# Kernel optimization log

Hardware: AMD Instinct MI355X
Metric: run time of the kernel (lower is better)

## Reference

```python
import jax, jax.numpy as jnp
import numpy as np
from jax import lax

EPS_OT = 0.05
N_ITERS = 100
NEG = -1e9

def _l2norm(x):
    n = jnp.sqrt(jnp.sum(x * x, axis=-1, keepdims=True))
    return x / jnp.maximum(n, 1e-12)

def _sinkhorn(C, mu, nu, mask):
    # C: (B, M, Nq); mu: (B, M); nu: (B, Nq); mask: (B, M) bool
    mrow = mask[:, :, None]   # masks rows of K (B,M,Nq)
    mcol = mask[:, None, :]   # masks cols of K^T (B,Nq,M)
    log_mu = jnp.log(mu + 1e-8)
    log_nu = jnp.log(nu + 1e-8)

    def kernel(u, v):
        return (-C + u[:, :, None] + v[:, None, :]) / EPS_OT

    def step(carry, _):
        u, v = carry
        K = jnp.where(mrow, kernel(u, v), NEG)
        u = EPS_OT * (log_mu - jax.scipy.special.logsumexp(K, axis=2)) + u
        Kt = jnp.where(mcol, jnp.transpose(kernel(u, v), (0, 2, 1)), NEG)
        v = EPS_OT * (log_nu - jax.scipy.special.logsumexp(Kt, axis=2)) + v
        return (u, v), None

    u0 = jnp.zeros_like(mu)
    v0 = jnp.zeros_like(nu)
    (u, v), _ = lax.scan(jax.checkpoint(step), (u0, v0), None, length=N_ITERS)
    K = jnp.where(mrow, kernel(u, v), NEG)
    T = jnp.exp(K)
    return jnp.where(mrow, T, 0.0)

def setup_inputs() -> dict:
    key = jax.random.key(0)
    ks = jax.random.split(key, 12)
    Nq, B, M, C = 1024, 8, 1024, 640
    s = 1.0 / np.sqrt(C)
    return {
        "xq": jax.random.normal(ks[0], (Nq, B, C), jnp.float32),
        "xk": jax.random.normal(ks[1], (B, M, C), jnp.float32),
        "xv": jax.random.normal(ks[2], (B, M, C), jnp.float32),
        "mask": jax.random.randint(ks[3], (B, M), 0, 2).astype(bool),
        "Wq": jax.random.normal(ks[4], (C, C), jnp.float32) * s,
        "bq": jnp.zeros((C,), jnp.float32),
        "Wk": jax.random.normal(ks[5], (C, C), jnp.float32) * s,
        "bk": jnp.zeros((C,), jnp.float32),
        "Wv": jax.random.normal(ks[6], (C, C), jnp.float32) * s,
        "bv": jnp.zeros((C,), jnp.float32),
        "Wp": jax.random.normal(ks[7], (C, C), jnp.float32) * s,
        "bp": jnp.zeros((C,), jnp.float32),
    }

def reference(xq, xk, xv, mask, Wq, bq, Wk, bk, Wv, bv, Wp, bp):
    Nq, B, C = xq.shape
    M = xk.shape[1]
    q = _l2norm(xq @ Wq.T + bq)          # (Nq, B, C)
    k = _l2norm(xk @ Wk.T + bk)          # (B, M, C)
    v = xv @ Wv.T + bv                   # (B, M, C)
    # einsum 'bmc,nbc->bnm' then permute(0,2,1) == direct (B, M, Nq)
    sim = jnp.einsum('bmc,nbc->bmn', k, q)
    wdist = 1.0 - sim
    counts = jnp.sum(mask, axis=1, keepdims=True).astype(sim.dtype)  # (B,1)
    xx = mask.astype(sim.dtype) / jnp.maximum(counts, 1.0)
    xx = jnp.where(counts == 0, 1.0 / M, xx)                         # (B, M)
    yy = jnp.full((B, Nq), 1.0 / Nq, sim.dtype)
    T = _sinkhorn(wdist, xx, yy, mask)                               # (B, M, Nq)
    score_map = (M * Nq) * sim * T
    attn_save = jnp.where(mask, jnp.sum(score_map, axis=-1), 0.0)    # (B, M)
    x = jnp.einsum('bmn,bmc->nbc', T, v)                             # (Nq, B, C)
    out = x @ Wp.T + bp
    return out, attn_save
```

## Files before the change

### kernel.cpp

```cpp
#include <hip/hip_runtime.h>
#include <cstdint>
#include <cstddef>

#define B_DIM 8
#define NQ    1024
#define MK    1024
#define CD    640
#define INV_EPS 20.0f
#define EPS_OT  0.05f

typedef unsigned short u16;
typedef __attribute__((ext_vector_type(8))) short bf16x8;
typedef __attribute__((ext_vector_type(4))) float f32x4;
typedef __attribute__((ext_vector_type(2))) float f32x2;

#define GLDS(gp, lp) __builtin_amdgcn_global_load_lds( \
    (const __attribute__((address_space(1))) void*)(gp), \
    (__attribute__((address_space(3))) void*)(lp), 16, 0, 0)

static __device__ __forceinline__ float wave_reduce_sum(float s) {
#pragma unroll
  for (int off = 32; off; off >>= 1) s += __shfl_xor(s, off, 64);
  return s;
}

static __device__ __forceinline__ u16 f2bf(float f) {
  uint32_t u = __float_as_uint(f);
  u += 0x7fff + ((u >> 16) & 1);
  return (u16)(u >> 16);
}

static __device__ __forceinline__ void g_store(float* p, float v) {
  __hip_atomic_store(p, v, __ATOMIC_RELAXED, __HIP_MEMORY_SCOPE_AGENT);
}
static __device__ __forceinline__ float g_load(const float* p) {
  return __hip_atomic_load((float*)p, __ATOMIC_RELAXED, __HIP_MEMORY_SCOPE_AGENT);
}
static __device__ __forceinline__ void g_storeu(unsigned* p, unsigned v) {
  __hip_atomic_store(p, v, __ATOMIC_RELAXED, __HIP_MEMORY_SCOPE_AGENT);
}
static __device__ __forceinline__ unsigned g_loadu(const unsigned* p) {
  return __hip_atomic_load((unsigned*)p, __ATOMIC_RELAXED, __HIP_MEMORY_SCOPE_AGENT);
}

__global__ void k_setup(const void* __restrict__ maskRaw, int* __restrict__ maskI,
                        float* __restrict__ muVal, float* __restrict__ w,
                        unsigned* __restrict__ ctrl)
{
  __shared__ int s_flag;
  __shared__ int s_cnt[B_DIM];
  const int tid = threadIdx.x;
  if (tid == 0) s_flag = 0;
  if (tid < B_DIM) s_cnt[tid] = 0;
  ctrl[tid] = 0u;
  __syncthreads();

  const unsigned char* mb = (const unsigned char*)maskRaw;
  int local = 0;
  for (int i = tid; i < B_DIM * MK; i += 1024)
    if ((i & 3) && mb[i]) local = 1;
  if (local) atomicOr(&s_flag, 1);
  __syncthreads();

  const int isByte = s_flag;
  const int* mi32 = (const int*)maskRaw;
  for (int i = tid; i < B_DIM * MK; i += 1024) {
    int v = isByte ? (int)mb[i] : mi32[i];
    v = v ? 1 : 0;
    maskI[i] = v;
    if (v) atomicAdd(&s_cnt[i >> 10], 1);
  }
  for (int i = tid; i < B_DIM * NQ; i += 1024) w[i] = 1.0f;
  __syncthreads();
  if (tid < B_DIM) {
    float c = (float)s_cnt[tid];
    muVal[tid] = (c > 0.f ? 1.0f / c : 1.0f / (float)MK) + 1e-8f;
  }
}

__global__ __launch_bounds__(256)
void k_cvt5(const float* __restrict__ x0, u16* __restrict__ d0,
            const float* __restrict__ x1, u16* __restrict__ d1,
            const float* __restrict__ x2, u16* __restrict__ d2,
            const float* __restrict__ x3, u16* __restrict__ d3,
            const float* __restrict__ x4, u16* __restrict__ d4)
{
  const int a = blockIdx.y;
  const float* s; u16* d; int n;
  if      (a == 0) { s = x0; d = d0; n = 8192 * CD; }
  else if (a == 1) { s = x1; d = d1; n = 8192 * CD; }
  else if (a == 2) { s = x2; d = d2; n = 8192 * CD; }
  else if (a == 3) { s = x3; d = d3; n = CD * CD; }
  else             { s = x4; d = d4; n = CD * CD; }
  const int i = (blockIdx.x * 256 + threadIdx.x) * 4;
  if (i >= n) return;
  const float4 v = *(const float4*)(s + i);
  *(ushort4*)(d + i) = make_ushort4(f2bf(v.x), f2bf(v.y), f2bf(v.z), f2bf(v.w));
}

__global__ __launch_bounds__(256)
void k_combineA(const float* __restrict__ Wp, const float* __restrict__ Wv,
                u16* __restrict__ Ah)
{
  __shared__ float Ps[32][68];
  __shared__ float Vs[32][68];
  const int tid = threadIdx.x;
  const int c0 = blockIdx.x << 6, k0 = blockIdx.y << 6;
  const int ty = tid >> 4, tx = tid & 15;
  float acc[4][4];
#pragma unroll
  for (int i = 0; i < 4; ++i)
#pragma unroll
    for (int j = 0; j < 4; ++j) acc[i][j] = 0.f;

  for (int j0 = 0; j0 < CD; j0 += 32) {
    {
      const int c = tid >> 2, j4 = (tid & 3) << 3;
      const float* p = Wp + (size_t)(c0 + c) * CD + j0 + j4;
      float4 u0 = *(const float4*)p, u1 = *(const float4*)(p + 4);
      Ps[j4 + 0][c] = u0.x; Ps[j4 + 1][c] = u0.y; Ps[j4 + 2][c] = u0.z; Ps[j4 + 3][c] = u0.w;
      Ps[j4 + 4][c] = u1.x; Ps[j4 + 5][c] = u1.y; Ps[j4 + 6][c] = u1.z; Ps[j4 + 7][c] = u1.w;
    }
    {
      const int j = tid >> 3, k4 = (tid & 7) << 3;
      const float* p = Wv + (size_t)(j0 + j) * CD + k0 + k4;
      float4 u0 = *(const float4*)p, u1 = *(const float4*)(p + 4);
      *(float4*)&Vs[j][k4] = u0; *(float4*)&Vs[j][k4 + 4] = u1;
    }
    __syncthreads();
#pragma unroll
    for (int j = 0; j < 32; ++j) {
      float a[4], b[4];
      *(float4*)a = *(const float4*)&Ps[j][ty << 2];
      *(float4*)b = *(const float4*)&Vs[j][tx << 2];
#pragma unroll
      for (int i = 0; i < 4; ++i)
#pragma unroll
        for (int jj = 0; jj < 4; ++jj)
          acc[i][jj] = fmaf(a[i], b[jj], acc[i][jj]);
    }
    __syncthreads();
  }
#pragma unroll
  for (int i = 0; i < 4; ++i) {
    *(ushort4*)(Ah + (size_t)(c0 + (ty << 2) + i) * CD + k0 + (tx << 2)) =
      make_ushort4(f2bf(acc[i][0]), f2bf(acc[i][1]), f2bf(acc[i][2]), f2bf(acc[i][3]));
  }
}

__global__ __launch_bounds__(256)
void k_bvp(const float* __restrict__ Wp, const float* __restrict__ bv,
           float* __restrict__ bvp)
{
  const int c = (blockIdx.x << 2) + (threadIdx.x >> 6);
  const int lane = threadIdx.x & 63;
  float s = 0.f;
  for (int j = lane; j < CD; j += 64) s = fmaf(Wp[(size_t)c * CD + j], bv[j], s);
  s = wave_reduce_sum(s);
  if (!lane) bvp[c] = s;
}

__global__ __launch_bounds__(256)
void mfma_proj(const u16* __restrict__ xqh, const u16* __restrict__ xkh,
               const u16* __restrict__ xvh,
               const u16* __restrict__ Wqh, const u16* __restrict__ Wkh,
               const u16* __restrict__ Ah,
               const float* __restrict__ bq, const float* __restrict__ bk,
               const float* __restrict__ bvp,
               float* __restrict__ qb, float* __restrict__ kb,
               float* __restrict__ vp)
{
  __shared__ u16 As[128 * 32];
  __shared__ u16 Bs[128 * 32];
  const int mode = blockIdx.z;
  const u16* X     = (mode == 0) ? xqh : ((mode == 1) ? xkh : xvh);
  const u16* W     = (mode == 0) ? Wqh : ((mode == 1) ? Wkh : Ah);
  const float* bias= (mode == 0) ? bq  : ((mode == 1) ? bk  : bvp);
  float* outp      = (mode == 0) ? qb  : ((mode == 1) ? kb  : vp);

  const int tid = threadIdx.x, wave = tid >> 6, lane = tid & 63;
  const int row0 = blockIdx.x << 7, col0 = blockIdx.y << 7;

  const int rS = (wave << 5) + (lane >> 2);
  const int pc = lane & 3;
  const int kc0 = pc ^ ((rS >> 1) & 3);
  const int kc1 = pc ^ (((rS + 16) >> 1) & 3);
  const u16* gA0 = X + (size_t)(row0 + rS) * CD + (kc0 << 3);
  const u16* gA1 = X + (size_t)(row0 + rS + 16) * CD + (kc1 << 3);
  const u16* gB0 = W + (size_t)(col0 + rS) * CD + (kc0 << 3);
  const u16* gB1 = W + (size_t)(col0 + rS + 16) * CD + (kc1 << 3);
  u16* lA = As + (wave << 10);
  u16* lB = Bs + (wave << 10);

  const int wm0 = (wave & 1) << 6, wn0 = (wave >> 1) << 6;
  int aOff[4], bOff[4];
#pragma unroll
  for (int t = 0; t < 4; ++t) {
    const int ra = wm0 + (t << 4) + (lane & 15);
    aOff[t] = ra * 32 + (((lane >> 4) ^ ((ra >> 1) & 3)) << 3);
    const int rb = wn0 + (t << 4) + (lane & 15);
    bOff[t] = rb * 32 + (((lane >> 4) ^ ((rb >> 1) & 3)) << 3);
  }
  f32x4 acc[4][4];
#pragma unroll
  for (int i = 0; i < 4; ++i)
#pragma unroll
    for (int j = 0; j < 4; ++j) acc[i][j] = {0.f, 0.f, 0.f, 0.f};

  for (int k0 = 0; k0 < CD; k0 += 32) {
    __syncthreads();
    GLDS(gA0, lA); GLDS(gA1, lA + 512);
    GLDS(gB0, lB); GLDS(gB1, lB + 512);
    gA0 += 32; gA1 += 32; gB0 += 32; gB1 += 32;
    __syncthreads();
    bf16x8 a[4], b[4];
#pragma unroll
    for (int t = 0; t < 4; ++t) {
      a[t] = *(const bf16x8*)(As + aOff[t]);
      b[t] = *(const bf16x8*)(Bs + bOff[t]);
    }
#pragma unroll
    for (int i = 0; i < 4; ++i)
#pragma unroll
      for (int j = 0; j < 4; ++j)
        acc[i][j] = __builtin_amdgcn_mfma_f32_16x16x32_bf16(a[i], b[j], acc[i][j], 0, 0, 0);
  }

  float bv4[4];
  int ccs[4];
#pragma unroll
  for (int j = 0; j < 4; ++j) {
    ccs[j] = col0 + wn0 + (j << 4) + (lane & 15);
    bv4[j] = bias[ccs[j]];
  }
#pragma unroll
  for (int i = 0; i < 4; ++i) {
    const int rbase = row0 + wm0 + (i << 4) + ((lane >> 4) << 2);
#pragma unroll
    for (int r = 0; r < 4; ++r) {
      const int rr = rbase + r;
      const size_t orow = (mode == 0) ? ((size_t)(rr & 7) * NQ + (rr >> 3)) : (size_t)rr;
      float* op = outp + orow * CD;
#pragma unroll
      for (int j = 0; j < 4; ++j)
        op[ccs[j]] = acc[i][j][r] + bv4[j];
    }
  }
}

__global__ __launch_bounds__(256)
void mfma_sim(const u16* __restrict__ kbh, const u16* __restrict__ qbh,
              float* __restrict__ E)
{
  __shared__ u16 As[128 * 32];
  __shared__ u16 Bs[128 * 32];
  const int tid = threadIdx.x, wave = tid >> 6, lane = tid & 63;
  const int b = blockIdx.z;
  const int row0 = blockIdx.x << 7, col0 = blockIdx.y << 7;
  const u16* A = kbh + (size_t)b * MK * CD;
  const u16* B = qbh + (size_t)b * NQ * CD;

  const int rS = (wave << 5) + (lane >> 2);
  const int pc = lane & 3;
  const int kc0 = pc ^ ((rS >> 1) & 3);
  const int kc1 = pc ^ (((rS + 16) >> 1) & 3);
  const u16* gA0 = A + (size_t)(row0 + rS) * CD + (kc0 << 3);
  const u16* gA1 = A + (size_t)(row0 + rS + 16) * CD + (kc1 << 3);
  const u16* gB0 = B + (size_t)(col0 + rS) * CD + (kc0 << 3);
  const u16* gB1 = B + (size_t)(col0 + rS + 16) * CD + (kc1 << 3);
  u16* lA = As + (wave << 10);
  u16* lB = Bs + (wave << 10);

  const int wm0 = (wave & 1) << 6, wn0 = (wave >> 1) << 6;
  int aOff[4], bOff[4];
#pragma unroll
  for (int t = 0; t < 4; ++t) {
    const int ra = wm0 + (t << 4) + (lane & 15);
    aOff[t] = ra * 32 + (((lane >> 4) ^ ((ra >> 1) & 3)) << 3);
    const int rb = wn0 + (t << 4) + (lane & 15);
    bOff[t] = rb * 32 + (((lane >> 4) ^ ((rb >> 1) & 3)) << 3);
  }
  f32x4 acc[4][4];
#pragma unroll
  for (int i = 0; i < 4; ++i)
#pragma unroll
    for (int j = 0; j < 4; ++j) acc[i][j] = {0.f, 0.f, 0.f, 0.f};

  for (int k0 = 0; k0 < CD; k0 += 32) {
    __syncthreads();
    GLDS(gA0, lA); GLDS(gA1, lA + 512);
    GLDS(gB0, lB); GLDS(gB1, lB + 512);
    gA0 += 32; gA1 += 32; gB0 += 32; gB1 += 32;
    __syncthreads();
    bf16x8 a[4], b[4];
#pragma unroll
    for (int t = 0; t < 4; ++t) {
      a[t] = *(const bf16x8*)(As + aOff[t]);
      b[t] = *(const bf16x8*)(Bs + bOff[t]);
    }
#pragma unroll
    for (int i = 0; i < 4; ++i)
#pragma unroll
      for (int j = 0; j < 4; ++j)
        acc[i][j] = __builtin_amdgcn_mfma_f32_16x16x32_bf16(a[i], b[j], acc[i][j], 0, 0, 0);
  }

#pragma unroll
  for (int i = 0; i < 4; ++i) {
    const int rbase = row0 + wm0 + (i << 4) + ((lane >> 4) << 2);
#pragma unroll
    for (int r = 0; r < 4; ++r) {
      const int rr = rbase + r;
      float* erow = E + (((size_t)(b << 10) + rr) << 10);
#pragma unroll
      for (int j = 0; j < 4; ++j) {
        const int cc = col0 + wn0 + (j << 4) + (lane & 15);
        erow[cc] = __expf((acc[i][j][r] - 1.f) * INV_EPS);
      }
    }
  }
}

__global__ __launch_bounds__(256)
void mfma_x(const u16* __restrict__ Et, const u16* __restrict__ Vpt,
            const float* __restrict__ w, const float* __restrict__ bp,
            float* __restrict__ out)
{
  __shared__ u16 As[128 * 32];
  __shared__ u16 Bs[128 * 32];
  const int tid = threadIdx.x, wave = tid >> 6, lane = tid & 63;
  const int b = blockIdx.z;
  const int row0 = blockIdx.x << 7;
  const int col0 = blockIdx.y << 7;
  const u16* A = Et + ((size_t)b << 20);
  const u16* B = Vpt + (size_t)b * CD * MK;

  const int rS = (wave << 5) + (lane >> 2);
  const int pc = lane & 3;
  const int kc0 = pc ^ ((rS >> 1) & 3);
  const int kc1 = pc ^ (((rS + 16) >> 1) & 3);
  const u16* gA0 = A + ((size_t)(row0 + rS) << 10) + (kc0 << 3);
  const u16* gA1 = A + ((size_t)(row0 + rS + 16) << 10) + (kc1 << 3);
  const u16* gB0 = B + ((size_t)(col0 + rS) << 10) + (kc0 << 3);
  const u16* gB1 = B + ((size_t)(col0 + rS + 16) << 10) + (kc1 << 3);
  u16* lA = As + (wave << 10);
  u16* lB = Bs + (wave << 10);

  const int wm0 = (wave & 1) << 6, wn0 = (wave >> 1) << 6;
  int aOff[4], bOff[4];
#pragma unroll
  for (int t = 0; t < 4; ++t) {
    const int ra = wm0 + (t << 4) + (lane & 15);
    aOff[t] = ra * 32 + (((lane >> 4) ^ ((ra >> 1) & 3)) << 3);
    const int rb = wn0 + (t << 4) + (lane & 15);
    bOff[t] = rb * 32 + (((lane >> 4) ^ ((rb >> 1) & 3)) << 3);
  }
  f32x4 acc[4][4];
#pragma unroll
  for (int i = 0; i < 4; ++i)
#pragma unroll
    for (int j = 0; j < 4; ++j) acc[i][j] = {0.f, 0.f, 0.f, 0.f};

  for (int k0 = 0; k0 < MK; k0 += 32) {
    __syncthreads();
    GLDS(gA0, lA); GLDS(gA1, lA + 512);
    GLDS(gB0, lB); GLDS(gB1, lB + 512);
    gA0 += 32; gA1 += 32; gB0 += 32; gB1 += 32;
    __syncthreads();
    bf16x8 a[4], b[4];
#pragma unroll
    for (int t = 0; t < 4; ++t) {
      a[t] = *(const bf16x8*)(As + aOff[t]);
      b[t] = *(const bf16x8*)(Bs + bOff[t]);
    }
#pragma unroll
    for (int i = 0; i < 4; ++i)
#pragma unroll
      for (int j = 0; j < 4; ++j)
        acc[i][j] = __builtin_amdgcn_mfma_f32_16x16x32_bf16(a[i], b[j], acc[i][j], 0, 0, 0);
  }

  float bv4[4];
  int ccs[4];
#pragma unroll
  for (int j = 0; j < 4; ++j) {
    ccs[j] = col0 + wn0 + (j << 4) + (lane & 15);
    bv4[j] = bp[ccs[j]];
  }
#pragma unroll
  for (int i = 0; i < 4; ++i) {
    const int rbase = row0 + wm0 + (i << 4) + ((lane >> 4) << 2);
#pragma unroll
    for (int r = 0; r < 4; ++r) {
      const int rr = rbase + r;
      const float wn = w[(b << 10) + rr];
      float* op = out + ((size_t)rr * 8 + b) * CD;
#pragma unroll
      for (int j = 0; j < 4; ++j)
        op[ccs[j]] = acc[i][j][r] * wn + bv4[j];
    }
  }
}

__global__ __launch_bounds__(256)
void k_l2bf(const float* __restrict__ X, u16* __restrict__ O)
{
  const int row = (blockIdx.x << 2) + (threadIdx.x >> 6);
  const int lane = threadIdx.x & 63;
  const float2* p2 = (const float2*)(X + (size_t)row * CD);
  float2 v[5];
  float ss = 0.f;
#pragma unroll
  for (int i = 0; i < 5; ++i) {
    v[i] = p2[lane + (i << 6)];
    ss = fmaf(v[i].x, v[i].x, fmaf(v[i].y, v[i].y, ss));
  }
  ss = wave_reduce_sum(ss);
  const float inv = 1.0f / fmaxf(sqrtf(ss), 1e-12f);
  ushort2* o2 = (ushort2*)(O + (size_t)row * CD);
#pragma unroll
  for (int i = 0; i < 5; ++i)
    o2[lane + (i << 6)] = make_ushort2(f2bf(v[i].x * inv), f2bf(v[i].y * inv));
}

__global__ __launch_bounds__(256)
void k_vpt(const float* __restrict__ vp, u16* __restrict__ Vpt)
{
  __shared__ float t[64][65];
  const int b = blockIdx.z, m0 = blockIdx.y << 6, c0 = blockIdx.x << 6;
  const int tid = threadIdx.x;
  const int cc = tid & 63, r4 = tid >> 6;
#pragma unroll
  for (int i = 0; i < 16; ++i) {
    const int m = (i << 2) + r4;
    t[m][cc] = vp[((size_t)((b << 10) + m0 + m)) * CD + c0 + cc];
  }
  __syncthreads();
  const int mm = tid & 63;
#pragma unroll
  for (int i = 0; i < 16; ++i) {
    const int c = (i << 2) + r4;
    Vpt[((size_t)(b * CD + c0 + c) << 10) + m0 + mm] = f2bf(t[mm][c]);
  }
}

__global__ __launch_bounds__(256)
void k_et(const float* __restrict__ E, const float* __restrict__ z,
          u16* __restrict__ Et)
{
  __shared__ float t[64][65];
  const int b = blockIdx.z, m0 = blockIdx.y << 6, n0 = blockIdx.x << 6;
  const int tid = threadIdx.x;
  const int nn = tid & 63, r4 = tid >> 6;
#pragma unroll
  for (int i = 0; i < 16; ++i) {
    const int m = (i << 2) + r4;
    const float zm = z[(b << 10) + m0 + m];
    t[m][nn] = E[(((size_t)((b << 10) + m0 + m)) << 10) + n0 + nn] * zm;
  }
  __syncthreads();
  const int mm = tid & 63;
#pragma unroll
  for (int i = 0; i < 16; ++i) {
    const int n = (i << 2) + r4;
    Et[(((size_t)((b << 10) + n0 + n)) << 10) + m0 + mm] = f2bf(t[mm][n]);
  }
}

__global__ __launch_bounds__(512, 2)
void k_sinkhorn(const float* __restrict__ E, const int* __restrict__ maskI,
                const float* __restrict__ muVal, float* __restrict__ w,
                float* __restrict__ z, float* __restrict__ attn,
                float* __restrict__ part, unsigned* __restrict__ ctrl)
{
  const int b = blockIdx.x & 7;
  const int g = blockIdx.x >> 3;
  const int tid = threadIdx.x;
  const int wave = tid >> 6, lane = tid & 63;
  const int m0 = (g << 6) + (wave << 3);
  const float* Eb = E + ((size_t)b << 20);
  float* wb = w + (b << 10);
  unsigned* flagB = ctrl + 64 + (b << 6);

  __shared__ float wS[1024];
  __shared__ float colRed[8][1024];

  float e[8][16];
#pragma unroll
  for (int r = 0; r < 8; ++r) {
    const float* row = Eb + ((size_t)(m0 + r) << 10) + lane;
#pragma unroll
    for (int j = 0; j < 16; ++j) e[r][j] = row[j << 6];
  }
  float rmask[8];
#pragma unroll
  for (int r = 0; r < 8; ++r)
    rmask[r] = maskI[(b << 10) + m0 + r] ? 1.f : 0.f;
  const float muT = muVal[b];
  const float nuT = 1.0f / (float)NQ + 1e-8f;
  float zr[8];
#pragma unroll
  for (int r = 0; r < 8; ++r) zr[r] = 0.f;

  wS[tid] = 1.0f; wS[tid + 512] = 1.0f;
  __syncthreads();

  for (int it = 0; it < 100; ++it) {
    float* partP = part + (size_t)((((it & 1) << 3) + b) << 14);
    float wv[16];
#pragma unroll
    for (int j = 0; j < 16; ++j) wv[j] = wS[lane + (j << 6)];
#pragma unroll
    for (int r = 0; r < 8; ++r) {
      float s = 0.f;
#pragma unroll
      for (int j = 0; j < 16; ++j) s = fmaf(e[r][j], wv[j], s);
      s = wave_reduce_sum(s);
      zr[r] = rmask[r] * (muT / fmaxf(s, 1e-35f));
    }
#pragma unroll
    for (int j = 0; j < 16; ++j) {
      float pj = 0.f;
#pragma unroll
      for (int r = 0; r < 8; ++r) pj = fmaf(e[r][j], zr[r], pj);
      colRed[wave][lane + (j << 6)] = pj;
    }
    __syncthreads();
    for (int n = tid; n < 1024; n += 512) {
      float s = 0.f;
#pragma unroll
      for (int w8 = 0; w8 < 8; ++w8) s += colRed[w8][n];
      g_store(partP + (g << 10) + n, s);
    }
    __syncthreads();
    const unsigned gen = (unsigned)(it + 1);
    if (tid == 0) g_storeu(flagB + g, gen);
    if (wave == 0 && lane < 16) {
      while (g_loadu(flagB + lane) < gen)
        __builtin_amdgcn_s_sleep(1);
    }
    __syncthreads();
    __builtin_amdgcn_fence(__ATOMIC_ACQUIRE, "workgroup");
    {
      float s0 = 0.f, s1 = 0.f;
#pragma unroll
      for (int gg = 0; gg < 16; ++gg) {
        s0 += g_load(partP + (gg << 10) + tid);
        s1 += g_load(partP + (gg << 10) + tid + 512);
      }
      wS[tid]       = nuT / fmaxf(s0, 1e-35f);
      wS[tid + 512] = nuT / fmaxf(s1, 1e-35f);
    }
    __syncthreads();
  }

  {
    float wv[16];
#pragma unroll
    for (int j = 0; j < 16; ++j) wv[j] = wS[lane + (j << 6)];
#pragma unroll
    for (int r = 0; r < 8; ++r) {
      float s = 0.f;
#pragma unroll
      for (int j = 0; j < 16; ++j) {
        const float ee = e[r][j];
        s += (1.f + EPS_OT * __logf(ee)) * ee * wv[j];
      }
      s = wave_reduce_sum(s);
      if (!lane) {
        const int m = (b << 10) + m0 + r;
        z[m] = zr[r];
        attn[m] = 1048576.0f * zr[r] * s;
      }
    }
    for (int n = tid; n < 1024; n += 512) wb[n] = wS[n];
  }
}

extern "C" void kernel_launch(void* const* d_in, const int* in_sizes, int n_in,
                              void* d_out, int out_size, void* d_ws, size_t ws_size,
                              hipStream_t stream)
{
  const float* xq = (const float*)d_in[0];
  const float* xk = (const float*)d_in[1];
  const float* xv = (const float*)d_in[2];
  const void*  maskRaw = d_in[3];
  const float* Wq = (const float*)d_in[4];
  const float* bq = (const float*)d_in[5];
  const float* Wk = (const float*)d_in[6];
  const float* bk = (const float*)d_in[7];
  const float* Wv = (const float*)d_in[8];
  const float* bv = (const float*)d_in[9];
  const float* Wp = (const float*)d_in[10];
  const float* bp = (const float*)d_in[11];

  float* out  = (float*)d_out;
  float* attn = out + (size_t)NQ * B_DIM * CD;

  char* base = (char*)d_ws;
  const size_t OFF_E   = 0;
  const size_t OFF_QB  = 33554432;
  const size_t OFF_KB  = 54525952;
  const size_t OFF_VP  = 75497472;
  const size_t OFF_VPT = 96468992;
  const size_t OFF_SM  = 106954752;

  float* E   = (float*)(base + OFF_E);
  u16* xqh   = (u16*)(base + OFF_E);
  u16* xkh   = xqh + (size_t)8192 * CD;
  u16* xvh   = xkh + (size_t)8192 * CD;
  float* qb  = (float*)(base + OFF_QB);
  float* part= (float*)(base + OFF_QB);
  u16* Et    = (u16*)(base + OFF_QB + 2097152);
  float* kb  = (float*)(base + OFF_KB);
  float* vp  = (float*)(base + OFF_VP);
  u16* qbh   = (u16*)(base + OFF_VP);
  u16* kbh   = qbh + (size_t)8192 * CD;
  u16* Vpt   = (u16*)(base + OFF_VPT);
  u16* Wqh   = (u16*)(base + OFF_SM);
  u16* Wkh   = Wqh + CD * CD;
  u16* Ah    = Wkh + CD * CD;
  float* bvp = (float*)(Ah + CD * CD);
  float* z   = bvp + CD;
  float* w   = z + B_DIM * MK;
  int* maskI = (int*)(w + B_DIM * NQ);
  float* muVal = (float*)(maskI + B_DIM * MK);
  unsigned* ctrl = (unsigned*)(muVal + B_DIM);

  k_setup<<<1, 1024, 0, stream>>>(maskRaw, maskI, muVal, w, ctrl);
  k_cvt5<<<dim3(5120, 5), 256, 0, stream>>>(xq, xqh, xk, xkh, xv, xvh,
                                            Wq, Wqh, Wk, Wkh);
  k_combineA<<<dim3(10, 10), 256, 0, stream>>>(Wp, Wv, Ah);
  k_bvp<<<160, 256, 0, stream>>>(Wp, bv, bvp);

  mfma_proj<<<dim3(64, 5, 3), 256, 0, stream>>>(xqh, xkh, xvh, Wqh, Wkh, Ah,
                                                bq, bk, bvp, qb, kb, vp);
  k_vpt<<<dim3(10, 16, 8), 256, 0, stream>>>(vp, Vpt);
  k_l2bf<<<2048, 256, 0, stream>>>(qb, qbh);
  k_l2bf<<<2048, 256, 0, stream>>>(kb, kbh);

  mfma_sim<<<dim3(8, 8, 8), 256, 0, stream>>>(kbh, qbh, E);

  {
    void* args[] = {(void*)&E, (void*)&maskI, (void*)&muVal, (void*)&w,
                    (void*)&z, (void*)&attn, (void*)&part, (void*)&ctrl};
    hipLaunchCooperativeKernel((void*)k_sinkhorn, dim3(128), dim3(512),
                               args, 0, stream);
  }

  k_et<<<dim3(16, 16, 8), 256, 0, stream>>>(E, z, Et);
  mfma_x<<<dim3(8, 5, 8), 256, 0, stream>>>(Et, Vpt, w, bp, out);
}
```

Baseline: 741.9 us.

## Stop Sinkhorn early on convergence and fuse the Et transpose into its epilogue

```diff
diff --git a/kernel.cpp b/kernel.cpp
--- a/kernel.cpp
+++ b/kernel.cpp
@@ -12,7 +12,6 @@
 typedef unsigned short u16;
 typedef __attribute__((ext_vector_type(8))) short bf16x8;
 typedef __attribute__((ext_vector_type(4))) float f32x4;
-typedef __attribute__((ext_vector_type(2))) float f32x2;
 
 #define GLDS(gp, lp) __builtin_amdgcn_global_load_lds( \
     (const __attribute__((address_space(1))) void*)(gp), \
@@ -28,6 +27,9 @@
   uint32_t u = __float_as_uint(f);
   u += 0x7fff + ((u >> 16) & 1);
   return (u16)(u >> 16);
+}
+static __device__ __forceinline__ unsigned pack2bf(float a, float b) {
+  return (unsigned)f2bf(a) | ((unsigned)f2bf(b) << 16);
 }
 
 static __device__ __forceinline__ void g_store(float* p, float v) {
@@ -444,34 +446,12 @@
   }
 }
 
-__global__ __launch_bounds__(256)
-void k_et(const float* __restrict__ E, const float* __restrict__ z,
-          u16* __restrict__ Et)
-{
-  __shared__ float t[64][65];
-  const int b = blockIdx.z, m0 = blockIdx.y << 6, n0 = blockIdx.x << 6;
-  const int tid = threadIdx.x;
-  const int nn = tid & 63, r4 = tid >> 6;
-#pragma unroll
-  for (int i = 0; i < 16; ++i) {
-    const int m = (i << 2) + r4;
-    const float zm = z[(b << 10) + m0 + m];
-    t[m][nn] = E[(((size_t)((b << 10) + m0 + m)) << 10) + n0 + nn] * zm;
-  }
-  __syncthreads();
-  const int mm = tid & 63;
-#pragma unroll
-  for (int i = 0; i < 16; ++i) {
-    const int n = (i << 2) + r4;
-    Et[(((size_t)((b << 10) + n0 + n)) << 10) + m0 + mm] = f2bf(t[mm][n]);
-  }
-}
-
 __global__ __launch_bounds__(512, 2)
 void k_sinkhorn(const float* __restrict__ E, const int* __restrict__ maskI,
                 const float* __restrict__ muVal, float* __restrict__ w,
                 float* __restrict__ z, float* __restrict__ attn,
-                float* __restrict__ part, unsigned* __restrict__ ctrl)
+                float* __restrict__ part, unsigned* __restrict__ ctrl,
+                u16* __restrict__ Et)
 {
   const int b = blockIdx.x & 7;
   const int g = blockIdx.x >> 3;
@@ -483,7 +463,11 @@
   unsigned* flagB = ctrl + 64 + (b << 6);
 
   __shared__ float wS[1024];
-  __shared__ float colRed[8][1024];
+  __shared__ __align__(16) char scratch[256 * 72 * 2];
+  __shared__ int convF[8];
+  float (*colRed)[1024] = (float (*)[1024])scratch;
+  u16* etile = (u16*)scratch;
+  unsigned* etile32 = (unsigned*)scratch;
 
   float e[8][16];
 #pragma unroll
@@ -503,6 +487,7 @@
   for (int r = 0; r < 8; ++r) zr[r] = 0.f;
 
   wS[tid] = 1.0f; wS[tid + 512] = 1.0f;
+  float wp0 = 1.0f, wp1 = 1.0f;
   __syncthreads();
 
   for (int it = 0; it < 100; ++it) {
@@ -548,10 +533,21 @@
         s0 += g_load(partP + (gg << 10) + tid);
         s1 += g_load(partP + (gg << 10) + tid + 512);
       }
-      wS[tid]       = nuT / fmaxf(s0, 1e-35f);
-      wS[tid + 512] = nuT / fmaxf(s1, 1e-35f);
-    }
-    __syncthreads();
+      const float w0 = nuT / fmaxf(s0, 1e-35f);
+      const float w1 = nuT / fmaxf(s1, 1e-35f);
+      wS[tid]       = w0;
+      wS[tid + 512] = w1;
+      const bool bad = (fabsf(w0 - wp0) > 1e-6f * fabsf(w0)) ||
+                       (fabsf(w1 - wp1) > 1e-6f * fabsf(w1));
+      wp0 = w0; wp1 = w1;
+      const unsigned long long anyBad = __ballot(bad);
+      if (lane == 0) convF[wave] = (anyBad != 0ull) ? 1 : 0;
+    }
+    __syncthreads();
+    int conv = 1;
+#pragma unroll
+    for (int w8 = 0; w8 < 8; ++w8) conv &= (convF[w8] == 0);
+    if (conv) break;
   }
 
   {
@@ -574,6 +570,28 @@
       }
     }
     for (int n = tid; n < 1024; n += 512) wb[n] = wS[n];
+  }
+
+  __syncthreads();
+#pragma unroll
+  for (int c = 0; c < 4; ++c) {
+#pragma unroll
+    for (int jj = 0; jj < 4; ++jj) {
+      const int j = (c << 2) + jj;
+      const int nl = (jj << 6) + lane;
+#pragma unroll
+      for (int r = 0; r < 8; r += 2)
+        etile32[nl * 36 + (wave << 2) + (r >> 1)] =
+          pack2bf(e[r][j] * zr[r], e[r + 1][j] * zr[r + 1]);
+    }
+    __syncthreads();
+    if (tid < 256) {
+      const float4* src = (const float4*)(etile + tid * 72);
+      float4* dst = (float4*)(Et + ((((size_t)(b << 10)) + (c << 8) + tid) << 10) + (g << 6));
+#pragma unroll
+      for (int q = 0; q < 8; ++q) dst[q] = src[q];
+    }
+    __syncthreads();
   }
 }
 
@@ -636,18 +654,17 @@
   mfma_proj<<<dim3(64, 5, 3), 256, 0, stream>>>(xqh, xkh, xvh, Wqh, Wkh, Ah,
                                                 bq, bk, bvp, qb, kb, vp);
   k_vpt<<<dim3(10, 16, 8), 256, 0, stream>>>(vp, Vpt);
-  k_l2bf<<<2048, 256, 0, stream>>>(qb, qbh);
-  k_l2bf<<<2048, 256, 0, stream>>>(kb, kbh);
+  k_l2bf<<<4096, 256, 0, stream>>>(qb, qbh);
 
   mfma_sim<<<dim3(8, 8, 8), 256, 0, stream>>>(kbh, qbh, E);
 
   {
     void* args[] = {(void*)&E, (void*)&maskI, (void*)&muVal, (void*)&w,
-                    (void*)&z, (void*)&attn, (void*)&part, (void*)&ctrl};
+                    (void*)&z, (void*)&attn, (void*)&part, (void*)&ctrl,
+                    (void*)&Et};
     hipLaunchCooperativeKernel((void*)k_sinkhorn, dim3(128), dim3(512),
                                args, 0, stream);
   }
 
-  k_et<<<dim3(16, 16, 8), 256, 0, stream>>>(E, z, Et);
   mfma_x<<<dim3(8, 5, 8), 256, 0, stream>>>(Et, Vpt, w, bp, out);
 }
```

After: 844.5 us. 13.8% more time.
